# Optimization experiments

Hardware: AMD Instinct MI355X
Metric: run time of the kernel (lower is better)

## Reference

```python
import jax, jax.numpy as jnp
import numpy as np


def setup_inputs() -> dict:
    key = jax.random.key(0)
    k1, k2 = jax.random.split(key)
    sat = jax.random.normal(k1, (96, 4, 64, 16), dtype=jnp.float32)
    grd = jax.random.normal(k2, (96, 4, 64, 16), dtype=jnp.float32)
    return {"sat_features": sat, "grd_features": grd}


def _corr(sat, grd):
    # sat: [Bs, h, W, c], grd: [Bg, h, Gw, c]
    Bs, h, W, c = sat.shape
    Bg, _, Gw, _ = grd.shape
    # circular pad along the width axis (dim 2), as in the torch code
    sat_pad = jnp.concatenate([sat, sat[:, :, : Gw - 1, :]], axis=2)  # [Bs,h,W+Gw-1,c]
    # torch flips grd along dim 3 (the c axis) before conv2d (cross-correlation)
    kern = grd[:, :, :, ::-1]  # [Bg,h,Gw,c] -> OIHW with O=Bg, I=h, H=Gw, W=c
    out = jax.lax.conv_general_dilated(
        sat_pad, kern, window_strides=(1, 1), padding='VALID',
        dimension_numbers=('NCHW', 'OIHW', 'NCHW'))  # [Bs,Bg,W,1]
    corr = out[..., 0]  # [Bs,Bg,W]
    orien = jnp.argmax(corr, axis=2).astype(jnp.int32)  # [Bs,Bg]
    return corr, orien


def reference(sat_features, grd_features):
    sat, grd = sat_features, grd_features
    Bs, h, W, c = sat.shape
    Bg, _, Gw, _ = grd.shape
    corr, orien = _corr(sat, grd)
    # per-pair circular shift + crop along width
    idx = (jnp.arange(Gw)[None, None, :] + orien[:, :, None]) % W  # [Bs,Bg,Gw]
    i_idx = jnp.arange(Bs)[:, None, None]  # broadcasts with idx
    sat_crop = sat[i_idx, :, idx, :]                # [Bs,Bg,Gw,h,c]
    sat_crop = jnp.transpose(sat_crop, (0, 1, 3, 2, 4))  # [Bs,Bg,h,Gw,c]
    norm = jnp.sqrt(jnp.sum(sat_crop ** 2, axis=(2, 3, 4), keepdims=True) + 1e-8)
    sat_matrix = sat_crop / norm
    dot = jnp.sum(sat_matrix * grd[None], axis=(2, 3, 4))  # [Bs,Bg]
    distance = 2.0 - 2.0 * dot.T                            # [Bg,Bs]
    return (sat_features, grd_features, distance, orien)
```

## Files before the change

### kernel.cpp

```cpp
#include <hip/hip_runtime.h>
#include <math.h>
#include <stdint.h>


#define BS   96
#define H    4
#define W    64
#define C    16
#define BG   96
#define HWC  (H*W*C)

#define SAT_ELEMS (BS*H*W*C)
#define OUT_DIST  (2*SAT_ELEMS)
#define OUT_ORIEN (OUT_DIST + BS*BG)

#define WS_NEEDED ((size_t)2 * SAT_ELEMS * 2)

typedef __attribute__((ext_vector_type(4)))  short short4v;
typedef __attribute__((ext_vector_type(8)))  short short8v;
typedef __attribute__((ext_vector_type(4)))  float f32x4;

__device__ __forceinline__ void bsplit(float x, unsigned short& hi, unsigned short& lo) {
    unsigned int u = __float_as_uint(x);
    unsigned int r = (u + 0x7FFFu + ((u >> 16) & 1u)) >> 16;
    hi = (unsigned short)r;
    float hf = __uint_as_float(r << 16);
    float l = x - hf;
    unsigned int ul = __float_as_uint(l);
    unsigned int rl = (ul + 0x7FFFu + ((ul >> 16) & 1u)) >> 16;
    lo = (unsigned short)rl;
}

__global__ __launch_bounds__(512)
void pf_pack_b(const float* __restrict__ sat, const float* __restrict__ grd,
               unsigned short* __restrict__ Bpk, float* __restrict__ out)
{
    int t = blockIdx.x * 512 + threadIdx.x;
    int lane = t & 63;
    int f    = t >> 6;
    int nt6  = f % 6;
    int g    = f / 6;
    int kh   = g & 1;
    int j    = g >> 1;

    int col = nt6 * 16 + (lane & 15);
    int u   = lane >> 4;
    int h   = kh * 2 + (u >> 1);
    int k0  = (u & 1) * 8;

    const float* row = grd + ((size_t)(col * 4 + h) * 64 + j) * 16 + (8 - k0);
    float tmp[8];
    *(float4*)&tmp[0] = *(const float4*)(row);
    *(float4*)&tmp[4] = *(const float4*)(row + 4);

    short8v hv, lv;
    #pragma unroll
    for (int e = 0; e < 8; ++e) {
        unsigned short hi, lo;
        bsplit(tmp[7 - e], hi, lo);
        hv[e] = (short)hi; lv[e] = (short)lo;
    }
    size_t base = (size_t)f << 10;
    *(short8v*)&Bpk[base + lane * 8]       = hv;
    *(short8v*)&Bpk[base + 512 + lane * 8] = lv;

    const float4* s4 = (const float4*)sat;
    const float4* g4 = (const float4*)grd;
    float4* o4 = (float4*)out;
    #pragma unroll
    for (int idx = t; idx < 2 * SAT_ELEMS / 4; idx += 49152) {
        o4[idx] = (idx < SAT_ELEMS / 4) ? s4[idx] : g4[idx - SAT_ELEMS / 4];
    }
}

#define MFMA16(a, b, c) __builtin_amdgcn_mfma_f32_16x16x32_bf16((a), (b), (c), 0, 0, 0)

__global__ __launch_bounds__(512, 4)
void pf_fused(const float* __restrict__ sat, const float* __restrict__ grd,
              const unsigned short* __restrict__ Bpk, float* __restrict__ out)
{
    __shared__ unsigned short sHi[4096], sLo[4096];
    __shared__ float corrPart[4][64][17];
    __shared__ float redW[8];
    __shared__ int   orienL[16];

    const int bs  = blockIdx.y;
    const int nt6 = blockIdx.x;
    const int bg0 = nt6 * 16;
    const int tid = threadIdx.x;
    const int wv  = tid >> 6, lane = tid & 63;
    const int u   = lane >> 4;
    const int mt2 = wv & 1;
    const int kq  = wv >> 1;

    {
        const float4* satB = (const float4*)(sat + (size_t)bs * HWC);
        float np = 0.f;
        #pragma unroll
        for (int t = tid; t < 1024; t += 512) {
            float4 v = satB[t];
            int e = 4 * t;
            int h = e >> 10, w = (e >> 4) & 63, k = e & 15;
            int cc = (h * 16 + k) >> 3;
            int dst = w * 64 + ((cc ^ (w & 7)) * 8) + (k & 7);
            short4v hvv, lvv;
            unsigned short hi, lo;
            bsplit(v.x, hi, lo); hvv[0] = hi; lvv[0] = lo;
            bsplit(v.y, hi, lo); hvv[1] = hi; lvv[1] = lo;
            bsplit(v.z, hi, lo); hvv[2] = hi; lvv[2] = lo;
            bsplit(v.w, hi, lo); hvv[3] = hi; lvv[3] = lo;
            *(short4v*)&sHi[dst] = hvv;
            *(short4v*)&sLo[dst] = lvv;
            np = fmaf(v.x, v.x, fmaf(v.y, v.y, fmaf(v.z, v.z, fmaf(v.w, v.w, np))));
        }
        #pragma unroll
        for (int off = 32; off; off >>= 1) np += __shfl_xor(np, off);
        if (lane == 0) redW[wv] = np;
    }
    __syncthreads();

    f32x4 acc0 = {0.f, 0.f, 0.f, 0.f};
    f32x4 acc1 = {0.f, 0.f, 0.f, 0.f};
    const int m0 = mt2 * 2;
    const int mbase0 = m0 * 16 + (lane & 15);
    const int laneB = lane * 8;
    const unsigned short* __restrict__ bbase = Bpk + ((size_t)nt6 << 10) + laneB;

    #pragma unroll 4
    for (int jj = 0; jj < 16; ++jj) {
        const int j = kq * 16 + jj;
        const unsigned short* bj = bbase + ((size_t)(j * 12) << 10);
        #pragma unroll
        for (int kh = 0; kh < 2; ++kh) {
            const unsigned short* bp = bj + ((size_t)(kh * 6) << 10);
            short8v bh = *(const short8v*)bp;
            short8v bl = *(const short8v*)(bp + 512);
            {
                const int r = (mbase0 + j) & 63;
                const int aoff = (r << 6) + ((((kh * 4 + u) ^ (r & 7))) << 3);
                short8v ah = *(const short8v*)&sHi[aoff];
                short8v al = *(const short8v*)&sLo[aoff];
                acc0 = MFMA16(ah, bh, acc0);
                acc0 = MFMA16(ah, bl, acc0);
                acc0 = MFMA16(al, bh, acc0);
                acc0 = MFMA16(al, bl, acc0);
            }
            {
                const int r = (mbase0 + 16 + j) & 63;
                const int aoff = (r << 6) + ((((kh * 4 + u) ^ (r & 7))) << 3);
                short8v ah = *(const short8v*)&sHi[aoff];
                short8v al = *(const short8v*)&sLo[aoff];
                acc1 = MFMA16(ah, bh, acc1);
                acc1 = MFMA16(ah, bl, acc1);
                acc1 = MFMA16(al, bh, acc1);
                acc1 = MFMA16(al, bl, acc1);
            }
        }
    }

    {
        const int gcol = lane & 15;
        const int rr0 = m0 * 16 + u * 4;
        #pragma unroll
        for (int reg = 0; reg < 4; ++reg) {
            corrPart[kq][rr0 + reg][gcol]      = acc0[reg];
            corrPart[kq][rr0 + 16 + reg][gcol] = acc1[reg];
        }
    }
    __syncthreads();

    #pragma unroll
    for (int t = 0; t < 2; ++t) {
        const int bgc = wv * 2 + t;
        float v = (corrPart[0][lane][bgc] + corrPart[1][lane][bgc])
                + (corrPart[2][lane][bgc] + corrPart[3][lane][bgc]);
        int idx = lane;
        #pragma unroll
        for (int off = 32; off; off >>= 1) {
            float ov = __shfl_xor(v, off);
            int   oi = __shfl_xor(idx, off);
            if (ov > v || (ov == v && oi < idx)) { v = ov; idx = oi; }
        }
        if (lane == 0) {
            orienL[bgc] = idx;
            out[OUT_ORIEN + bs * BG + bg0 + bgc] = (float)idx;
        }
    }
    __syncthreads();

    const float nrm = sqrtf(((redW[0] + redW[1]) + (redW[2] + redW[3]))
                          + ((redW[4] + redW[5]) + (redW[6] + redW[7])) + 1e-8f);

    #pragma unroll
    for (int t = 0; t < 2; ++t) {
        const int bgc = wv * 2 + t;
        const int bg = bg0 + bgc;
        const int r = (lane + orienL[bgc]) & 63;
        float s = 0.f;
        #pragma unroll
        for (int h = 0; h < 4; ++h) {
            const float4* sp = (const float4*)&sat[(((size_t)bs * 4 + h) * 64 + r) * 16];
            const float4* gp = (const float4*)&grd[(((size_t)bg * 4 + h) * 64 + lane) * 16];
            #pragma unroll
            for (int c4 = 0; c4 < 4; ++c4) {
                float4 sv = sp[c4];
                float4 gv = gp[c4];
                s = fmaf(sv.x, gv.x, fmaf(sv.y, gv.y, fmaf(sv.z, gv.z, fmaf(sv.w, gv.w, s))));
            }
        }
        #pragma unroll
        for (int off = 32; off; off >>= 1) s += __shfl_xor(s, off);
        if (lane == 0)
            out[OUT_DIST + (size_t)bg * BS + bs] = 2.f - 2.f * (s / nrm);
    }
}

__device__ __forceinline__ int satIdxFB(int hw, int c4) {
    return hw * 16 + 4 * ((c4 + (hw >> 1)) & 3);
}
__device__ __forceinline__ float rot_add(int baddr, float p) {
    return __int_as_float(__builtin_amdgcn_ds_bpermute(baddr, __float_as_int(p)));
}
__device__ __forceinline__ float dot_rev(const float4 s0, const float4 s1,
                                         const float4 s2, const float4 s3,
                                         const float* __restrict__ g) {
    float p0 = fmaf(s0.x, g[15], fmaf(s0.y, g[14], fmaf(s0.z, g[13], s0.w * g[12])));
    float p1 = fmaf(s1.x, g[11], fmaf(s1.y, g[10], fmaf(s1.z, g[ 9], s1.w * g[ 8])));
    float p2 = fmaf(s2.x, g[ 7], fmaf(s2.y, g[ 6], fmaf(s2.z, g[ 5], s2.w * g[ 4])));
    float p3 = fmaf(s3.x, g[ 3], fmaf(s3.y, g[ 2], fmaf(s3.z, g[ 1], s3.w * g[ 0])));
    return (p0 + p1) + (p2 + p3);
}
#define NB 8
__global__ __launch_bounds__(256)
void pf_fused_fb(const float* __restrict__ sat, const float* __restrict__ grd,
                 float* __restrict__ out)
{
    __shared__ float satL[H * W * C];
    __shared__ float partL[NB * 4 * W];
    __shared__ float sumL[4];
    __shared__ float dotP[NB * 4];
    __shared__ int   orienL[NB];
    const int bs = blockIdx.y, bg0 = blockIdx.x * NB;
    const int tid = threadIdx.x, wv = tid >> 6, lane = tid & 63;
    const float4* sp = (const float4*)(sat + (((size_t)bs * H + wv) * W + lane) * C);
    const float4 s0 = sp[0], s1 = sp[1], s2 = sp[2], s3 = sp[3];
    { const int hw = wv * W + lane;
      *(float4*)&satL[satIdxFB(hw,0)] = s0; *(float4*)&satL[satIdxFB(hw,1)] = s1;
      *(float4*)&satL[satIdxFB(hw,2)] = s2; *(float4*)&satL[satIdxFB(hw,3)] = s3; }
    { float a = fmaf(s0.x,s0.x,fmaf(s0.y,s0.y,fmaf(s0.z,s0.z,s0.w*s0.w)));
      float b = fmaf(s1.x,s1.x,fmaf(s1.y,s1.y,fmaf(s1.z,s1.z,s1.w*s1.w)));
      float c = fmaf(s2.x,s2.x,fmaf(s2.y,s2.y,fmaf(s2.z,s2.z,s2.w*s2.w)));
      float d = fmaf(s3.x,s3.x,fmaf(s3.y,s3.y,fmaf(s3.z,s3.z,s3.w*s3.w)));
      float s = (a+b)+(c+d);
      #pragma unroll
      for (int off = 32; off; off >>= 1) s += __shfl_xor(s, off);
      if (lane == 0) sumL[wv] = s; }
    const float* gpB = grd + (size_t)(bg0 * H + wv) * W * C;
    #pragma unroll
    for (int bp = 0; bp < NB/2; ++bp) {
        const float* gA = gpB + (2*bp) * HWC;
        const float* gB2 = gpB + (2*bp+1) * HWC;
        float accA = 0.f, accB = 0.f;
        int baddr = lane << 2;
        #pragma unroll 2
        for (int j = 0; j < W; ++j) {
            float pA = dot_rev(s0,s1,s2,s3, gA + j*C);
            float pB = dot_rev(s0,s1,s2,s3, gB2 + j*C);
            accA += rot_add(baddr, pA); accB += rot_add(baddr, pB);
            baddr = (baddr + 4) & 255;
        }
        partL[((2*bp)*4 + wv)*W + lane] = accA;
        partL[((2*bp+1)*4 + wv)*W + lane] = accB;
    }
    __syncthreads();
    for (int b = wv; b < NB; b += 4) {
        float v = (partL[(b*4+0)*W+lane] + partL[(b*4+1)*W+lane])
                + (partL[(b*4+2)*W+lane] + partL[(b*4+3)*W+lane]);
        int idx = lane;
        #pragma unroll
        for (int off = 32; off; off >>= 1) {
            float ov = __shfl_xor(v, off); int oi = __shfl_xor(idx, off);
            if (ov > v || (ov == v && oi < idx)) { v = ov; idx = oi; }
        }
        if (lane == 0) { orienL[b] = idx; out[OUT_ORIEN + bs*BG + (bg0+b)] = (float)idx; }
    }
    __syncthreads();
    const float nrm = sqrtf(sumL[0]+sumL[1]+sumL[2]+sumL[3] + 1e-8f);
    { float dp[NB];
      #pragma unroll
      for (int b = 0; b < NB; ++b) {
          const int row = (lane + orienL[b]) & 63;
          const float* gRow = grd + (((size_t)(bg0+b)*H + wv)*W + lane)*C;
          float s = 0.f;
          #pragma unroll
          for (int c4 = 0; c4 < 4; ++c4) {
              float4 sv = *(const float4*)&satL[satIdxFB(wv*W+row, c4)];
              float4 gv = *(const float4*)(gRow + 4*c4);
              s = fmaf(sv.x,gv.x, fmaf(sv.y,gv.y, fmaf(sv.z,gv.z, fmaf(sv.w,gv.w, s))));
          }
          dp[b] = s;
      }
      #pragma unroll
      for (int b = 0; b < NB; ++b) {
          float s = dp[b];
          #pragma unroll
          for (int off = 32; off; off >>= 1) s += __shfl_xor(s, off);
          if (lane == 0) dotP[b*4 + wv] = s;
      } }
    __syncthreads();
    if (tid < NB) {
        float d = ((dotP[tid*4+0]+dotP[tid*4+1])+(dotP[tid*4+2]+dotP[tid*4+3])) / nrm;
        out[OUT_DIST + (size_t)(bg0+tid)*BS + bs] = 2.f - 2.f*d;
    }
}

extern "C" void kernel_launch(void* const* d_in, const int* in_sizes, int n_in,
                              void* d_out, int out_size, void* d_ws, size_t ws_size,
                              hipStream_t stream) {
    const float* sat = (const float*)d_in[0];
    const float* grd = (const float*)d_in[1];
    float* out = (float*)d_out;

    if (ws_size < WS_NEEDED) {
        hipMemcpyAsync(out,             sat, (size_t)SAT_ELEMS * sizeof(float),
                       hipMemcpyDeviceToDevice, stream);
        hipMemcpyAsync(out + SAT_ELEMS, grd, (size_t)SAT_ELEMS * sizeof(float),
                       hipMemcpyDeviceToDevice, stream);
        dim3 grid(BG / NB, BS);
        pf_fused_fb<<<grid, 256, 0, stream>>>(sat, grd, out);
        return;
    }

    unsigned short* Bpk = (unsigned short*)d_ws;
    pf_pack_b<<<96, 512, 0, stream>>>(sat, grd, Bpk, out);
    pf_fused<<<dim3(6, BS), 512, 0, stream>>>(sat, grd, Bpk, out);
}
```

Before: 49.65 us.

## Split correlation K-loop across all 8 waves with full M tile and B prefetch

Each wave now owns all four 16-row M tiles and one eighth of the reduction range, instead of two M tiles and a quarter of the range. Each B fragment loaded from global memory is reused across four MFMA tiles rather than two, and the next iteration's B fragments are loaded ahead so global latency overlaps the MFMA work. The cost is more accumulator registers, double-buffered B registers and a larger shared partial-sum buffer (8 partials). The final reduction also sums eight partials instead of four, which changes the floating-point summation order.

Measured after the change: 48.99 us. About the same (-1.3%).

```diff
diff --git a/kernel.cpp b/kernel.cpp
--- a/kernel.cpp
+++ b/kernel.cpp
@@ -80,7 +80,7 @@
               const unsigned short* __restrict__ Bpk, float* __restrict__ out)
 {
     __shared__ unsigned short sHi[4096], sLo[4096];
-    __shared__ float corrPart[4][64][17];
+    __shared__ float corrPart[8][64][17];
     __shared__ float redW[8];
     __shared__ int   orienL[16];
 
@@ -90,8 +90,7 @@
     const int tid = threadIdx.x;
     const int wv  = tid >> 6, lane = tid & 63;
     const int u   = lane >> 4;
-    const int mt2 = wv & 1;
-    const int kq  = wv >> 1;
+    const int kq  = wv;
 
     {
         const float4* satB = (const float4*)(sat + (size_t)bs * HWC);
@@ -119,52 +118,60 @@
     }
     __syncthreads();
 
-    f32x4 acc0 = {0.f, 0.f, 0.f, 0.f};
-    f32x4 acc1 = {0.f, 0.f, 0.f, 0.f};
-    const int m0 = mt2 * 2;
-    const int mbase0 = m0 * 16 + (lane & 15);
-    const int laneB = lane * 8;
-    const unsigned short* __restrict__ bbase = Bpk + ((size_t)nt6 << 10) + laneB;
-
-    #pragma unroll 4
-    for (int jj = 0; jj < 16; ++jj) {
-        const int j = kq * 16 + jj;
-        const unsigned short* bj = bbase + ((size_t)(j * 12) << 10);
-        #pragma unroll
-        for (int kh = 0; kh < 2; ++kh) {
-            const unsigned short* bp = bj + ((size_t)(kh * 6) << 10);
-            short8v bh = *(const short8v*)bp;
-            short8v bl = *(const short8v*)(bp + 512);
-            {
-                const int r = (mbase0 + j) & 63;
-                const int aoff = (r << 6) + ((((kh * 4 + u) ^ (r & 7))) << 3);
-                short8v ah = *(const short8v*)&sHi[aoff];
-                short8v al = *(const short8v*)&sLo[aoff];
-                acc0 = MFMA16(ah, bh, acc0);
-                acc0 = MFMA16(ah, bl, acc0);
-                acc0 = MFMA16(al, bh, acc0);
-                acc0 = MFMA16(al, bl, acc0);
-            }
-            {
-                const int r = (mbase0 + 16 + j) & 63;
-                const int aoff = (r << 6) + ((((kh * 4 + u) ^ (r & 7))) << 3);
-                short8v ah = *(const short8v*)&sHi[aoff];
-                short8v al = *(const short8v*)&sLo[aoff];
-                acc1 = MFMA16(ah, bh, acc1);
-                acc1 = MFMA16(ah, bl, acc1);
-                acc1 = MFMA16(al, bh, acc1);
-                acc1 = MFMA16(al, bl, acc1);
-            }
-        }
-    }
+    f32x4 acc0 = {0.f,0.f,0.f,0.f}, acc1 = {0.f,0.f,0.f,0.f};
+    f32x4 acc2 = {0.f,0.f,0.f,0.f}, acc3 = {0.f,0.f,0.f,0.f};
+
+    const int l15 = lane & 15;
+    const unsigned short* __restrict__ bb =
+        Bpk + (((size_t)(kq * 8 * 2) * 6 + nt6) << 10) + lane * 8;
+
+    short8v bh0 = *(const short8v*)(bb);
+    short8v bl0 = *(const short8v*)(bb + 512);
+    short8v bh1 = *(const short8v*)(bb + (6 << 10));
+    short8v bl1 = *(const short8v*)(bb + (6 << 10) + 512);
+
+    #define MT_STEP(ACC, mnum, J, BH0, BL0, BH1, BL1) { \
+        const int r_ = ((mnum) * 16 + l15 + (J)) & 63; \
+        const int base_ = r_ << 6; \
+        const int rs_ = r_ & 7; \
+        { const int aoff_ = base_ + (((u) ^ rs_) << 3); \
+          short8v ah_ = *(const short8v*)&sHi[aoff_]; \
+          short8v al_ = *(const short8v*)&sLo[aoff_]; \
+          ACC = MFMA16(ah_, BH0, ACC); ACC = MFMA16(ah_, BL0, ACC); \
+          ACC = MFMA16(al_, BH0, ACC); ACC = MFMA16(al_, BL0, ACC); } \
+        { const int aoff_ = base_ + ((((4 + u)) ^ rs_) << 3); \
+          short8v ah_ = *(const short8v*)&sHi[aoff_]; \
+          short8v al_ = *(const short8v*)&sLo[aoff_]; \
+          ACC = MFMA16(ah_, BH1, ACC); ACC = MFMA16(ah_, BL1, ACC); \
+          ACC = MFMA16(al_, BH1, ACC); ACC = MFMA16(al_, BL1, ACC); } }
+
+    #pragma unroll
+    for (int jj = 0; jj < 8; ++jj) {
+        const int j = kq * 8 + jj;
+        short8v nh0, nl0, nh1, nl1;
+        if (jj < 7) {
+            const unsigned short* nb = bb + (size_t)(jj + 1) * (12 << 10);
+            nh0 = *(const short8v*)(nb);
+            nl0 = *(const short8v*)(nb + 512);
+            nh1 = *(const short8v*)(nb + (6 << 10));
+            nl1 = *(const short8v*)(nb + (6 << 10) + 512);
+        }
+        MT_STEP(acc0, 0, j, bh0, bl0, bh1, bl1);
+        MT_STEP(acc1, 1, j, bh0, bl0, bh1, bl1);
+        MT_STEP(acc2, 2, j, bh0, bl0, bh1, bl1);
+        MT_STEP(acc3, 3, j, bh0, bl0, bh1, bl1);
+        if (jj < 7) { bh0 = nh0; bl0 = nl0; bh1 = nh1; bl1 = nl1; }
+    }
+    #undef MT_STEP
 
     {
-        const int gcol = lane & 15;
-        const int rr0 = m0 * 16 + u * 4;
+        const int rr = u * 4;
         #pragma unroll
         for (int reg = 0; reg < 4; ++reg) {
-            corrPart[kq][rr0 + reg][gcol]      = acc0[reg];
-            corrPart[kq][rr0 + 16 + reg][gcol] = acc1[reg];
+            corrPart[kq][rr + reg][l15]      = acc0[reg];
+            corrPart[kq][16 + rr + reg][l15] = acc1[reg];
+            corrPart[kq][32 + rr + reg][l15] = acc2[reg];
+            corrPart[kq][48 + rr + reg][l15] = acc3[reg];
         }
     }
     __syncthreads();
@@ -172,8 +179,10 @@
     #pragma unroll
     for (int t = 0; t < 2; ++t) {
         const int bgc = wv * 2 + t;
-        float v = (corrPart[0][lane][bgc] + corrPart[1][lane][bgc])
-                + (corrPart[2][lane][bgc] + corrPart[3][lane][bgc]);
+        float v = ((corrPart[0][lane][bgc] + corrPart[1][lane][bgc])
+                +  (corrPart[2][lane][bgc] + corrPart[3][lane][bgc]))
+                + ((corrPart[4][lane][bgc] + corrPart[5][lane][bgc])
+                +  (corrPart[6][lane][bgc] + corrPart[7][lane][bgc]));
         int idx = lane;
         #pragma unroll
         for (int off = 32; off; off >>= 1) {
```

## Split fused correlation kernel into M-half correlation and separate epilogue kernel

Applied to the files above, without the earlier changes.

The fused kernel becomes three kernels. The pack kernel now also computes per-satellite norms. A correlation kernel is launched over a grid with twice as many blocks, each covering half the width shifts, and writes partial (max, index) pairs to workspace. A third kernel merges the two halves, writes the orientation and computes the normalized distance. The aim is more parallelism and occupancy in the MFMA stage, and the MFMA accumulation is split into two chains to shorten dependency stalls. In exchange it adds a kernel launch, workspace round-trips, and a second satellite load and bf16 split per block.

Result: slower. 57.54 us (+15.9%).

```diff
diff --git a/kernel.cpp b/kernel.cpp
--- a/kernel.cpp
+++ b/kernel.cpp
@@ -14,7 +14,9 @@
 #define OUT_DIST  (2*SAT_ELEMS)
 #define OUT_ORIEN (OUT_DIST + BS*BG)
 
-#define WS_NEEDED ((size_t)2 * SAT_ELEMS * 2)
+#define WS_MI_OFF   ((size_t)2 * SAT_ELEMS * 2)
+#define WS_NORM_OFF (WS_MI_OFF + (size_t)BS * BG * 2 * 2 * 4)
+#define WS_NEEDED   (WS_NORM_OFF + 512)
 
 typedef __attribute__((ext_vector_type(4)))  short short4v;
 typedef __attribute__((ext_vector_type(8)))  short short8v;
@@ -33,73 +35,99 @@
 
 __global__ __launch_bounds__(512)
 void pf_pack_b(const float* __restrict__ sat, const float* __restrict__ grd,
-               unsigned short* __restrict__ Bpk, float* __restrict__ out)
+               unsigned short* __restrict__ Bpk, float* __restrict__ norms,
+               float* __restrict__ out)
 {
-    int t = blockIdx.x * 512 + threadIdx.x;
-    int lane = t & 63;
-    int f    = t >> 6;
-    int nt6  = f % 6;
-    int g    = f / 6;
-    int kh   = g & 1;
-    int j    = g >> 1;
-
-    int col = nt6 * 16 + (lane & 15);
-    int u   = lane >> 4;
-    int h   = kh * 2 + (u >> 1);
-    int k0  = (u & 1) * 8;
-
-    const float* row = grd + ((size_t)(col * 4 + h) * 64 + j) * 16 + (8 - k0);
-    float tmp[8];
-    *(float4*)&tmp[0] = *(const float4*)(row);
-    *(float4*)&tmp[4] = *(const float4*)(row + 4);
-
-    short8v hv, lv;
-    #pragma unroll
-    for (int e = 0; e < 8; ++e) {
-        unsigned short hi, lo;
-        bsplit(tmp[7 - e], hi, lo);
-        hv[e] = (short)hi; lv[e] = (short)lo;
-    }
-    size_t base = (size_t)f << 10;
-    *(short8v*)&Bpk[base + lane * 8]       = hv;
-    *(short8v*)&Bpk[base + 512 + lane * 8] = lv;
-
-    const float4* s4 = (const float4*)sat;
-    const float4* g4 = (const float4*)grd;
-    float4* o4 = (float4*)out;
-    #pragma unroll
-    for (int idx = t; idx < 2 * SAT_ELEMS / 4; idx += 49152) {
-        o4[idx] = (idx < SAT_ELEMS / 4) ? s4[idx] : g4[idx - SAT_ELEMS / 4];
+    __shared__ float nred[8];
+    const int tid = threadIdx.x;
+    const int t = blockIdx.x * 512 + tid;
+
+    {
+        int lane = t & 63;
+        int f    = t >> 6;
+        int nt6  = f % 6;
+        int g    = f / 6;
+        int kh   = g & 1;
+        int j    = g >> 1;
+
+        int col = nt6 * 16 + (lane & 15);
+        int u   = lane >> 4;
+        int h   = kh * 2 + (u >> 1);
+        int k0  = (u & 1) * 8;
+
+        const float* row = grd + ((size_t)(col * 4 + h) * 64 + j) * 16 + (8 - k0);
+        float tmp[8];
+        *(float4*)&tmp[0] = *(const float4*)(row);
+        *(float4*)&tmp[4] = *(const float4*)(row + 4);
+
+        short8v hv, lv;
+        #pragma unroll
+        for (int e = 0; e < 8; ++e) {
+            unsigned short hi, lo;
+            bsplit(tmp[7 - e], hi, lo);
+            hv[e] = (short)hi; lv[e] = (short)lo;
+        }
+        size_t base = (size_t)f << 10;
+        *(short8v*)&Bpk[base + lane * 8]       = hv;
+        *(short8v*)&Bpk[base + 512 + lane * 8] = lv;
+    }
+
+    {
+        const int wv = tid >> 6, lane = tid & 63;
+        float np = 0.f;
+        const float4* sb = (const float4*)(sat + (size_t)blockIdx.x * HWC);
+        #pragma unroll
+        for (int x = tid; x < 1024; x += 512) {
+            float4 v = sb[x];
+            np = fmaf(v.x, v.x, fmaf(v.y, v.y, fmaf(v.z, v.z, fmaf(v.w, v.w, np))));
+        }
+        #pragma unroll
+        for (int off = 32; off; off >>= 1) np += __shfl_xor(np, off);
+        if (lane == 0) nred[wv] = np;
+        __syncthreads();
+        if (tid == 0) {
+            float s = ((nred[0] + nred[1]) + (nred[2] + nred[3]))
+                    + ((nred[4] + nred[5]) + (nred[6] + nred[7]));
+            norms[blockIdx.x] = sqrtf(s + 1e-8f);
+        }
+    }
+
+    {
+        const float4* s4 = (const float4*)sat;
+        const float4* g4 = (const float4*)grd;
+        float4* o4 = (float4*)out;
+        #pragma unroll
+        for (int idx = t; idx < 2 * SAT_ELEMS / 4; idx += 49152) {
+            o4[idx] = (idx < SAT_ELEMS / 4) ? s4[idx] : g4[idx - SAT_ELEMS / 4];
+        }
     }
 }
 
 #define MFMA16(a, b, c) __builtin_amdgcn_mfma_f32_16x16x32_bf16((a), (b), (c), 0, 0, 0)
 
-__global__ __launch_bounds__(512, 4)
-void pf_fused(const float* __restrict__ sat, const float* __restrict__ grd,
-              const unsigned short* __restrict__ Bpk, float* __restrict__ out)
+__global__ __launch_bounds__(512, 8)
+void pf_corrm(const float* __restrict__ sat, const unsigned short* __restrict__ Bpk,
+              float* __restrict__ mi)
 {
     __shared__ unsigned short sHi[4096], sLo[4096];
-    __shared__ float corrPart[4][64][17];
-    __shared__ float redW[8];
-    __shared__ int   orienL[16];
-
+    __shared__ float corrPart[4][32][17];
+
+    const int nt6 = blockIdx.x;
     const int bs  = blockIdx.y;
-    const int nt6 = blockIdx.x;
+    const int mh  = blockIdx.z;
     const int bg0 = nt6 * 16;
     const int tid = threadIdx.x;
     const int wv  = tid >> 6, lane = tid & 63;
-    const int u   = lane >> 4;
-    const int mt2 = wv & 1;
+    const int u   = lane >> 4, l15 = lane & 15, l31 = lane & 31;
+    const int mt  = wv & 1;
     const int kq  = wv >> 1;
 
     {
         const float4* satB = (const float4*)(sat + (size_t)bs * HWC);
-        float np = 0.f;
-        #pragma unroll
-        for (int t = tid; t < 1024; t += 512) {
-            float4 v = satB[t];
-            int e = 4 * t;
+        #pragma unroll
+        for (int x = tid; x < 1024; x += 512) {
+            float4 v = satB[x];
+            int e = 4 * x;
             int h = e >> 10, w = (e >> 4) & 63, k = e & 15;
             int cc = (h * 16 + k) >> 3;
             int dst = w * 64 + ((cc ^ (w & 7)) * 8) + (k & 7);
@@ -111,91 +139,89 @@
             bsplit(v.w, hi, lo); hvv[3] = hi; lvv[3] = lo;
             *(short4v*)&sHi[dst] = hvv;
             *(short4v*)&sLo[dst] = lvv;
-            np = fmaf(v.x, v.x, fmaf(v.y, v.y, fmaf(v.z, v.z, fmaf(v.w, v.w, np))));
-        }
-        #pragma unroll
-        for (int off = 32; off; off >>= 1) np += __shfl_xor(np, off);
-        if (lane == 0) redW[wv] = np;
-    }
-    __syncthreads();
-
-    f32x4 acc0 = {0.f, 0.f, 0.f, 0.f};
-    f32x4 acc1 = {0.f, 0.f, 0.f, 0.f};
-    const int m0 = mt2 * 2;
-    const int mbase0 = m0 * 16 + (lane & 15);
-    const int laneB = lane * 8;
-    const unsigned short* __restrict__ bbase = Bpk + ((size_t)nt6 << 10) + laneB;
+        }
+    }
+    __syncthreads();
+
+    f32x4 c0 = {0.f,0.f,0.f,0.f}, c1 = {0.f,0.f,0.f,0.f};
+    const int m = mh * 2 + mt;
+    const int mbase = m * 16 + l15;
 
     #pragma unroll 4
     for (int jj = 0; jj < 16; ++jj) {
         const int j = kq * 16 + jj;
-        const unsigned short* bj = bbase + ((size_t)(j * 12) << 10);
+        const int r = (mbase + j) & 63;
+        const int arow = r << 6;
+        const int rsw = r & 7;
         #pragma unroll
         for (int kh = 0; kh < 2; ++kh) {
-            const unsigned short* bp = bj + ((size_t)(kh * 6) << 10);
+            const unsigned short* bp =
+                Bpk + (((size_t)((j * 2 + kh) * 6 + nt6)) << 10) + lane * 8;
             short8v bh = *(const short8v*)bp;
             short8v bl = *(const short8v*)(bp + 512);
-            {
-                const int r = (mbase0 + j) & 63;
-                const int aoff = (r << 6) + ((((kh * 4 + u) ^ (r & 7))) << 3);
-                short8v ah = *(const short8v*)&sHi[aoff];
-                short8v al = *(const short8v*)&sLo[aoff];
-                acc0 = MFMA16(ah, bh, acc0);
-                acc0 = MFMA16(ah, bl, acc0);
-                acc0 = MFMA16(al, bh, acc0);
-                acc0 = MFMA16(al, bl, acc0);
-            }
-            {
-                const int r = (mbase0 + 16 + j) & 63;
-                const int aoff = (r << 6) + ((((kh * 4 + u) ^ (r & 7))) << 3);
-                short8v ah = *(const short8v*)&sHi[aoff];
-                short8v al = *(const short8v*)&sLo[aoff];
-                acc1 = MFMA16(ah, bh, acc1);
-                acc1 = MFMA16(ah, bl, acc1);
-                acc1 = MFMA16(al, bh, acc1);
-                acc1 = MFMA16(al, bl, acc1);
-            }
-        }
-    }
-
-    {
-        const int gcol = lane & 15;
-        const int rr0 = m0 * 16 + u * 4;
-        #pragma unroll
-        for (int reg = 0; reg < 4; ++reg) {
-            corrPart[kq][rr0 + reg][gcol]      = acc0[reg];
-            corrPart[kq][rr0 + 16 + reg][gcol] = acc1[reg];
-        }
+            const int cc = kh * 4 + u;
+            const int aoff = arow + ((cc ^ rsw) << 3);
+            short8v ah = *(const short8v*)&sHi[aoff];
+            short8v al = *(const short8v*)&sLo[aoff];
+            c0 = MFMA16(ah, bh, c0);
+            c1 = MFMA16(ah, bl, c1);
+            c1 = MFMA16(al, bh, c1);
+            c0 = MFMA16(al, bl, c0);
+        }
+    }
+    f32x4 acc = c0 + c1;
+
+    {
+        const int rr = mt * 16 + u * 4;
+        #pragma unroll
+        for (int reg = 0; reg < 4; ++reg)
+            corrPart[kq][rr + reg][l15] = acc[reg];
     }
     __syncthreads();
 
     #pragma unroll
     for (int t = 0; t < 2; ++t) {
         const int bgc = wv * 2 + t;
-        float v = (corrPart[0][lane][bgc] + corrPart[1][lane][bgc])
-                + (corrPart[2][lane][bgc] + corrPart[3][lane][bgc]);
-        int idx = lane;
-        #pragma unroll
-        for (int off = 32; off; off >>= 1) {
+        float v = (corrPart[0][l31][bgc] + corrPart[1][l31][bgc])
+                + (corrPart[2][l31][bgc] + corrPart[3][l31][bgc]);
+        int idx = mh * 32 + l31;
+        #pragma unroll
+        for (int off = 16; off; off >>= 1) {
             float ov = __shfl_xor(v, off);
             int   oi = __shfl_xor(idx, off);
             if (ov > v || (ov == v && oi < idx)) { v = ov; idx = oi; }
         }
         if (lane == 0) {
-            orienL[bgc] = idx;
-            out[OUT_ORIEN + bs * BG + bg0 + bgc] = (float)idx;
-        }
-    }
-    __syncthreads();
-
-    const float nrm = sqrtf(((redW[0] + redW[1]) + (redW[2] + redW[3]))
-                          + ((redW[4] + redW[5]) + (redW[6] + redW[7])) + 1e-8f);
+            float2 p = make_float2(v, (float)idx);
+            *(float2*)&mi[((size_t)(bs * BG + bg0 + bgc) * 2 + mh) * 2] = p;
+        }
+    }
+}
+
+__global__ __launch_bounds__(512)
+void pf_epim(const float* __restrict__ sat, const float* __restrict__ grd,
+             const float* __restrict__ mi, const float* __restrict__ norms,
+             float* __restrict__ out)
+{
+    const int nt6 = blockIdx.x;
+    const int bs  = blockIdx.y;
+    const int bg0 = nt6 * 16;
+    const int tid = threadIdx.x;
+    const int wv  = tid >> 6, lane = tid & 63;
+
+    const float nrm = norms[bs];
 
     #pragma unroll
     for (int t = 0; t < 2; ++t) {
-        const int bgc = wv * 2 + t;
-        const int bg = bg0 + bgc;
-        const int r = (lane + orienL[bgc]) & 63;
+        const int bg = bg0 + wv * 2 + t;
+        float2 p0 = *(const float2*)&mi[((size_t)(bs * BG + bg) * 2 + 0) * 2];
+        float2 p1 = *(const float2*)&mi[((size_t)(bs * BG + bg) * 2 + 1) * 2];
+        const float idxf = (p0.x >= p1.x) ? p0.y : p1.y;
+        const int orien = (int)idxf;
+        if (lane == 0)
+            out[OUT_ORIEN + bs * BG + bg] = idxf;
+
+        const int r = (lane + orien) & 63;
         float s = 0.f;
         #pragma unroll
         for (int h = 0; h < 4; ++h) {
@@ -331,7 +357,11 @@
         return;
     }
 
-    unsigned short* Bpk = (unsigned short*)d_ws;
-    pf_pack_b<<<96, 512, 0, stream>>>(sat, grd, Bpk, out);
-    pf_fused<<<dim3(6, BS), 512, 0, stream>>>(sat, grd, Bpk, out);
-}
+    unsigned short* Bpk   = (unsigned short*)d_ws;
+    float*          mi    = (float*)((char*)d_ws + WS_MI_OFF);
+    float*          norms = (float*)((char*)d_ws + WS_NORM_OFF);
+
+    pf_pack_b<<<96, 512, 0, stream>>>(sat, grd, Bpk, norms, out);
+    pf_corrm<<<dim3(6, BS, 2), 512, 0, stream>>>(sat, Bpk, mi);
+    pf_epim<<<dim3(6, BS), 512, 0, stream>>>(sat, grd, mi, norms, out);
+}
```
